# Kernel optimization log

Hardware: AMD Instinct MI355X
Metric: run time of the kernel (lower is better)

## Reference

```python
import jax, jax.numpy as jnp
import numpy as np


def setup_inputs() -> dict:
    key = jax.random.key(0)
    k1, k2 = jax.random.split(key)
    Q, C, S, D = 16384, 2048, 5, 512
    x = jax.random.normal(k1, (Q, D), dtype=jnp.float32)
    y = jax.random.normal(k2, (C, S, D), dtype=jnp.float32)
    return {"x": x, "y": y}


def reference(x, y):
    # x: [Q, D] queries; y: [C, S, D] support sets per class
    Q = x.shape[0]
    x = x.reshape(Q, -1)                       # [Q, D]
    C, S = y.shape[0], y.shape[1]
    y_proto = y.reshape(C, S, -1).mean(axis=1)  # [C, D] class prototypes
    # pairwise dot products (the nested loop in the original), then row softmax
    d = jnp.einsum('qd,cd->qc', x, y_proto)     # [Q, C]
    return jax.nn.softmax(d, axis=1)
```

## Files before the change

kernel.cpp:

```cpp
#include <hip/hip_runtime.h>
#include <hip/hip_bf16.h>
#include <math.h>

#define QTOT 16384
#define CDIM 2048
#define DDIM 512
#define SDIM 5

#define NKT   (DDIM / 32)
#define NCTG  (CDIM / 16)
#define MB    32
#define NT    1024
#define NWAVE 16
#define CPW   (CDIM / NWAVE)
#define CTPW  (CPW / 16)

typedef short  s8v  __attribute__((ext_vector_type(8)));
typedef float  f32x4 __attribute__((ext_vector_type(4)));

__device__ __forceinline__ unsigned short f2bf(float f) {
  unsigned int u = __float_as_uint(f);
  return (unsigned short)((u + 0x7FFFu + ((u >> 16) & 1u)) >> 16);
}
__device__ __forceinline__ float bf2f(unsigned short h) {
  return __uint_as_float(((unsigned int)h) << 16);
}

__global__ void __launch_bounds__(256)
prep_kernel(const float* __restrict__ y, unsigned short* __restrict__ bf) {
  const int t  = threadIdx.x;
  const int c0 = blockIdx.x * 8;
  #pragma unroll
  for (int e = 0; e < 16; ++e) {
    int flat = e * 256 + t;
    int cl   = flat >> 9;
    int k    = flat & 511;
    int c    = c0 + cl;
    const float* p = y + (size_t)c * (SDIM * DDIM) + k;
    float s = 0.f;
    #pragma unroll
    for (int ss = 0; ss < SDIM; ++ss) s += p[ss * DDIM];
    float v  = s * 0.2f;
    unsigned short hi = f2bf(v);
    unsigned short lo = f2bf(v - bf2f(hi));
    int kt   = k >> 5;
    int ctg  = c >> 4;
    int lane = (c & 15) + 16 * ((k & 31) >> 3);
    int j    = k & 7;
    size_t base = ((size_t)(kt * NCTG + ctg) * 2) * 512 + lane * 8 + j;
    bf[base]       = hi;
    bf[base + 512] = lo;
  }
}

#define MFMA __builtin_amdgcn_mfma_f32_16x16x32_bf16
#define GRP(ci, B0, B1, B2, B3) \
  acc[0][ci]   = MFMA(ah0, B0, acc[0][ci],   0,0,0); \
  acc[1][ci]   = MFMA(ah1, B0, acc[1][ci],   0,0,0); \
  acc[0][ci]   = MFMA(al0, B0, acc[0][ci],   0,0,0); \
  acc[1][ci]   = MFMA(al1, B0, acc[1][ci],   0,0,0); \
  acc[0][ci]   = MFMA(ah0, B1, acc[0][ci],   0,0,0); \
  acc[1][ci]   = MFMA(ah1, B1, acc[1][ci],   0,0,0); \
  acc[0][ci+1] = MFMA(ah0, B2, acc[0][ci+1], 0,0,0); \
  acc[1][ci+1] = MFMA(ah1, B2, acc[1][ci+1], 0,0,0); \
  acc[0][ci+1] = MFMA(al0, B2, acc[0][ci+1], 0,0,0); \
  acc[1][ci+1] = MFMA(al1, B2, acc[1][ci+1], 0,0,0); \
  acc[0][ci+1] = MFMA(ah0, B3, acc[0][ci+1], 0,0,0); \
  acc[1][ci+1] = MFMA(ah1, B3, acc[1][ci+1], 0,0,0);

#define LOADG(A_, B_, C_, D_, base, ci0) \
  A_ = B8[(base) + (ci0) * 128];       \
  B_ = B8[(base) + (ci0) * 128 + 64];  \
  C_ = B8[(base) + (ci0) * 128 + 128]; \
  D_ = B8[(base) + (ci0) * 128 + 192];

__global__ void __launch_bounds__(NT, 4)
gemm_softmax_kernel(const float* __restrict__ x,
                    const unsigned short* __restrict__ bf,
                    float* __restrict__ out) {
  __shared__ unsigned short ldsA[32768];

  const int t    = threadIdx.x;
  const int lane = t & 63;
  const int w    = t >> 6;
  const int q0   = blockIdx.x * MB;

  {
    const float4* x4 = (const float4*)(x + (size_t)q0 * DDIM);
    #pragma unroll
    for (int i = 0; i < 4; ++i) {
      int idx = t + NT * i;
      int q   = idx >> 7;
      int k4  = idx & 127;
      float4 f = x4[(size_t)q * 128 + k4];
      int kt    = k4 >> 3;
      int mt    = q >> 4;
      int lanea = (q & 15) + 16 * ((k4 >> 1) & 3);
      int j0    = (k4 & 1) * 4;
      unsigned short h0 = f2bf(f.x), h1 = f2bf(f.y), h2 = f2bf(f.z), h3 = f2bf(f.w);
      unsigned short l0 = f2bf(f.x - bf2f(h0)), l1 = f2bf(f.y - bf2f(h1));
      unsigned short l2 = f2bf(f.z - bf2f(h2)), l3 = f2bf(f.w - bf2f(h3));
      ushort4* dh = (ushort4*)&ldsA[((kt * 4 + mt * 2 + 0) * 512) + lanea * 8 + j0];
      ushort4* dl = (ushort4*)&ldsA[((kt * 4 + mt * 2 + 1) * 512) + lanea * 8 + j0];
      *dh = make_ushort4(h0, h1, h2, h3);
      *dl = make_ushort4(l0, l1, l2, l3);
    }
  }
  __syncthreads();

  f32x4 acc[2][CTPW];
  #pragma unroll
  for (int mt = 0; mt < 2; ++mt)
    #pragma unroll
    for (int ci = 0; ci < CTPW; ++ci) acc[mt][ci] = (f32x4)0.f;

  const s8v* A8 = (const s8v*)ldsA;
  const s8v* B8 = (const s8v*)bf;

  int bb = (w * CTPW) * 2 * 64 + lane;
  s8v P0, P1, P2, P3, Q0, Q1, Q2, Q3;
  LOADG(P0, P1, P2, P3, bb, 0);
  #pragma unroll 1
  for (int kt = 0; kt < NKT; ++kt) {
    const int kb = kt * 4 * 64 + lane;
    s8v ah0 = A8[kb];
    s8v al0 = A8[kb + 64];
    s8v ah1 = A8[kb + 128];
    s8v al1 = A8[kb + 192];
    LOADG(Q0, Q1, Q2, Q3, bb, 2);
    GRP(0, P0, P1, P2, P3);
    LOADG(P0, P1, P2, P3, bb, 4);
    GRP(2, Q0, Q1, Q2, Q3);
    LOADG(Q0, Q1, Q2, Q3, bb, 6);
    GRP(4, P0, P1, P2, P3);
    const int bbn = (((kt + 1) & 15) * NCTG + w * CTPW) * 2 * 64 + lane;
    LOADG(P0, P1, P2, P3, bbn, 0);
    GRP(6, Q0, Q1, Q2, Q3);
    bb = bbn;
  }
  __syncthreads();

  float* red = (float*)ldsA;
  const int g  = lane >> 4;
  const int cl = lane & 15;

  float mx[2][4];
  #pragma unroll
  for (int mt = 0; mt < 2; ++mt)
    #pragma unroll
    for (int r = 0; r < 4; ++r) {
      float v = acc[mt][0][r];
      #pragma unroll
      for (int ci = 1; ci < CTPW; ++ci) v = fmaxf(v, acc[mt][ci][r]);
      #pragma unroll
      for (int off = 1; off < 16; off <<= 1) v = fmaxf(v, __shfl_xor(v, off, 64));
      mx[mt][r] = v;
    }
  if (cl == 0) {
    #pragma unroll
    for (int mt = 0; mt < 2; ++mt)
      #pragma unroll
      for (int r = 0; r < 4; ++r) red[(mt * 16 + g * 4 + r) * NWAVE + w] = mx[mt][r];
  }
  __syncthreads();
  #pragma unroll
  for (int mt = 0; mt < 2; ++mt)
    #pragma unroll
    for (int r = 0; r < 4; ++r) {
      float v = red[(mt * 16 + g * 4 + r) * NWAVE + cl];
      #pragma unroll
      for (int off = 1; off < 16; off <<= 1) v = fmaxf(v, __shfl_xor(v, off, 64));
      mx[mt][r] = v;
    }
  __syncthreads();

  float sm[2][4];
  #pragma unroll
  for (int mt = 0; mt < 2; ++mt)
    #pragma unroll
    for (int r = 0; r < 4; ++r) {
      float s = 0.f;
      #pragma unroll
      for (int ci = 0; ci < CTPW; ++ci) {
        float e = __expf(acc[mt][ci][r] - mx[mt][r]);
        acc[mt][ci][r] = e;
        s += e;
      }
      #pragma unroll
      for (int off = 1; off < 16; off <<= 1) s += __shfl_xor(s, off, 64);
      sm[mt][r] = s;
    }
  if (cl == 0) {
    #pragma unroll
    for (int mt = 0; mt < 2; ++mt)
      #pragma unroll
      for (int r = 0; r < 4; ++r) red[512 + (mt * 16 + g * 4 + r) * NWAVE + w] = sm[mt][r];
  }
  __syncthreads();

  #pragma unroll
  for (int mt = 0; mt < 2; ++mt)
    #pragma unroll
    for (int r = 0; r < 4; ++r) {
      float s = red[512 + (mt * 16 + g * 4 + r) * NWAVE + cl];
      #pragma unroll
      for (int off = 1; off < 16; off <<= 1) s += __shfl_xor(s, off, 64);
      float inv = 1.0f / s;
      size_t row = (size_t)(q0 + mt * 16 + g * 4 + r) * CDIM + w * CPW + cl;
      #pragma unroll
      for (int ci = 0; ci < CTPW; ++ci)
        out[row + ci * 16] = acc[mt][ci][r] * inv;
    }
}

extern "C" void kernel_launch(void* const* d_in, const int* in_sizes, int n_in,
                              void* d_out, int out_size, void* d_ws, size_t ws_size,
                              hipStream_t stream) {
  const float* x = (const float*)d_in[0];
  const float* y = (const float*)d_in[1];
  float* out     = (float*)d_out;
  unsigned short* bf = (unsigned short*)d_ws;

  hipLaunchKernelGGL(prep_kernel, dim3(256), dim3(256), 0, stream, y, bf);
  hipLaunchKernelGGL(gemm_softmax_kernel, dim3(QTOT / MB), dim3(NT), 0, stream,
                     x, bf, out);
}
```

Measured before the change: 265.5 us.

## Use 8 waves with 16 column tiles each and a deeper B-register prefetch pipeline

Halves the block to 512 threads (8 waves), so each wave covers 256 classes (16 column tiles) and reuses its A fragments across twice as many MFMAs. The B-operand load pipeline grows from two to four register buffer sets, with byte-offset addressing, sched_barrier and s_setprio around each MFMA group to keep loads issued ahead of compute. The softmax reductions are adjusted for 8 waves. The trade-off is much higher register pressure from 32 accumulators plus 16 prefetch vectors per lane, which may lower occupancy or cause spills.

Result: no change. 261.7 us (-1.4%).

```diff
diff --git a/kernel.cpp b/kernel.cpp
--- a/kernel.cpp
+++ b/kernel.cpp
@@ -7,15 +7,15 @@
 #define DDIM 512
 #define SDIM 5
 
-#define NKT   (DDIM / 32)
-#define NCTG  (CDIM / 16)
+#define NKT   16
+#define NCTG  128
 #define MB    32
-#define NT    1024
-#define NWAVE 16
-#define CPW   (CDIM / NWAVE)
-#define CTPW  (CPW / 16)
-
-typedef short  s8v  __attribute__((ext_vector_type(8)));
+#define NT    512
+#define NWAVE 8
+#define CPW   256
+#define CTPW  16
+
+typedef short  s8v   __attribute__((ext_vector_type(8)));
 typedef float  f32x4 __attribute__((ext_vector_type(4)));
 
 __device__ __forceinline__ unsigned short f2bf(float f) {
@@ -68,27 +68,37 @@
   acc[0][ci+1] = MFMA(ah0, B3, acc[0][ci+1], 0,0,0); \
   acc[1][ci+1] = MFMA(ah1, B3, acc[1][ci+1], 0,0,0);
 
-#define LOADG(A_, B_, C_, D_, base, ci0) \
-  A_ = B8[(base) + (ci0) * 128];       \
-  B_ = B8[(base) + (ci0) * 128 + 64];  \
-  C_ = B8[(base) + (ci0) * 128 + 128]; \
-  D_ = B8[(base) + (ci0) * 128 + 192];
-
-__global__ void __launch_bounds__(NT, 4)
+#define LOADB(A_, B_, C_, D_, off) do {              \
+    const char* p_ = wb + (off);                     \
+    A_ = *(const s8v*)(p_ + lane16);                 \
+    B_ = *(const s8v*)(p_ + lane16 + 1024);          \
+    C_ = *(const s8v*)(p_ + lane16 + 2048);          \
+    D_ = *(const s8v*)(p_ + lane16 + 3072);          \
+  } while (0)
+
+#define PHASE(L0, L1, L2, L3, loff, ci, C0, C1, C2, C3) \
+  LOADB(L0, L1, L2, L3, loff);                          \
+  __builtin_amdgcn_sched_barrier(0);                    \
+  __builtin_amdgcn_s_setprio(1);                        \
+  GRP(ci, C0, C1, C2, C3);                              \
+  __builtin_amdgcn_s_setprio(0);
+
+__global__ void __launch_bounds__(NT, 2)
 gemm_softmax_kernel(const float* __restrict__ x,
                     const unsigned short* __restrict__ bf,
                     float* __restrict__ out) {
   __shared__ unsigned short ldsA[32768];
 
-  const int t    = threadIdx.x;
-  const int lane = t & 63;
-  const int w    = t >> 6;
-  const int q0   = blockIdx.x * MB;
+  const int t      = threadIdx.x;
+  const int lane   = t & 63;
+  const int w      = __builtin_amdgcn_readfirstlane(t >> 6);
+  const int lane16 = lane * 16;
+  const int q0     = blockIdx.x * MB;
 
   {
     const float4* x4 = (const float4*)(x + (size_t)q0 * DDIM);
     #pragma unroll
-    for (int i = 0; i < 4; ++i) {
+    for (int i = 0; i < 8; ++i) {
       int idx = t + NT * i;
       int q   = idx >> 7;
       int k4  = idx & 127;
@@ -115,11 +125,14 @@
     for (int ci = 0; ci < CTPW; ++ci) acc[mt][ci] = (f32x4)0.f;
 
   const s8v* A8 = (const s8v*)ldsA;
-  const s8v* B8 = (const s8v*)bf;
-
-  int bb = (w * CTPW) * 2 * 64 + lane;
-  s8v P0, P1, P2, P3, Q0, Q1, Q2, Q3;
-  LOADG(P0, P1, P2, P3, bb, 0);
+  const char* wb = (const char*)bf + w * 32768;
+
+  s8v P0,P1,P2,P3, Q0,Q1,Q2,Q3, R0,R1,R2,R3, S0,S1,S2,S3;
+  unsigned cur = 0, nxt = 262144;
+  LOADB(P0,P1,P2,P3, cur + 0);
+  LOADB(Q0,Q1,Q2,Q3, cur + 4096);
+  LOADB(R0,R1,R2,R3, cur + 8192);
+
   #pragma unroll 1
   for (int kt = 0; kt < NKT; ++kt) {
     const int kb = kt * 4 * 64 + lane;
@@ -127,16 +140,16 @@
     s8v al0 = A8[kb + 64];
     s8v ah1 = A8[kb + 128];
     s8v al1 = A8[kb + 192];
-    LOADG(Q0, Q1, Q2, Q3, bb, 2);
-    GRP(0, P0, P1, P2, P3);
-    LOADG(P0, P1, P2, P3, bb, 4);
-    GRP(2, Q0, Q1, Q2, Q3);
-    LOADG(Q0, Q1, Q2, Q3, bb, 6);
-    GRP(4, P0, P1, P2, P3);
-    const int bbn = (((kt + 1) & 15) * NCTG + w * CTPW) * 2 * 64 + lane;
-    LOADG(P0, P1, P2, P3, bbn, 0);
-    GRP(6, Q0, Q1, Q2, Q3);
-    bb = bbn;
+    PHASE(S0,S1,S2,S3, cur + 12288,  0, P0,P1,P2,P3);
+    PHASE(P0,P1,P2,P3, cur + 16384,  2, Q0,Q1,Q2,Q3);
+    PHASE(Q0,Q1,Q2,Q3, cur + 20480,  4, R0,R1,R2,R3);
+    PHASE(R0,R1,R2,R3, cur + 24576,  6, S0,S1,S2,S3);
+    PHASE(S0,S1,S2,S3, cur + 28672,  8, P0,P1,P2,P3);
+    PHASE(P0,P1,P2,P3, nxt + 0,     10, Q0,Q1,Q2,Q3);
+    PHASE(Q0,Q1,Q2,Q3, nxt + 4096,  12, R0,R1,R2,R3);
+    PHASE(R0,R1,R2,R3, nxt + 8192,  14, S0,S1,S2,S3);
+    cur = nxt;
+    nxt = (unsigned)((kt + 2) & 15) * 262144u;
   }
   __syncthreads();
 
@@ -167,9 +180,9 @@
   for (int mt = 0; mt < 2; ++mt)
     #pragma unroll
     for (int r = 0; r < 4; ++r) {
-      float v = red[(mt * 16 + g * 4 + r) * NWAVE + cl];
-      #pragma unroll
-      for (int off = 1; off < 16; off <<= 1) v = fmaxf(v, __shfl_xor(v, off, 64));
+      float v = red[(mt * 16 + g * 4 + r) * NWAVE + (cl & 7)];
+      #pragma unroll
+      for (int off = 1; off < 8; off <<= 1) v = fmaxf(v, __shfl_xor(v, off, 64));
       mx[mt][r] = v;
     }
   __syncthreads();
@@ -194,17 +207,17 @@
     #pragma unroll
     for (int mt = 0; mt < 2; ++mt)
       #pragma unroll
-      for (int r = 0; r < 4; ++r) red[512 + (mt * 16 + g * 4 + r) * NWAVE + w] = sm[mt][r];
-  }
-  __syncthreads();
-
-  #pragma unroll
-  for (int mt = 0; mt < 2; ++mt)
-    #pragma unroll
-    for (int r = 0; r < 4; ++r) {
-      float s = red[512 + (mt * 16 + g * 4 + r) * NWAVE + cl];
-      #pragma unroll
-      for (int off = 1; off < 16; off <<= 1) s += __shfl_xor(s, off, 64);
+      for (int r = 0; r < 4; ++r) red[256 + (mt * 16 + g * 4 + r) * NWAVE + w] = sm[mt][r];
+  }
+  __syncthreads();
+
+  #pragma unroll
+  for (int mt = 0; mt < 2; ++mt)
+    #pragma unroll
+    for (int r = 0; r < 4; ++r) {
+      float s = red[256 + (mt * 16 + g * 4 + r) * NWAVE + (cl & 7)];
+      #pragma unroll
+      for (int off = 1; off < 8; off <<= 1) s += __shfl_xor(s, off, 64);
       float inv = 1.0f / s;
       size_t row = (size_t)(q0 + mt * 16 + g * 4 + r) * CDIM + w * CPW + cl;
       #pragma unroll
```
